# Kernel tuning notes

Measured on AMD Instinct MI355X. Metric: run time of the kernel, lower is better.

## Reference

```python
import jax, jax.numpy as jnp
import numpy as np

# MQIF constants (match init_kwargs / torch defaults)
A = 0.04
B = 0.2
VR = -60.0
VT = -40.0
V_RESET = -60.0
V_PEAK = 30.0
D = 2.0
TAU_M = 10.0
TAU_U = 100.0
DT = 0.05


def setup_inputs() -> dict:
    key = jax.random.key(0)
    input_current = jax.random.normal(key, (16, 4096, 512), dtype=jnp.float32)
    return {"input_current": input_current}


def reference(input_current):
    # input_current: [batch, steps, features]
    batch, steps, features = input_current.shape
    dtype = input_current.dtype
    v0 = jnp.full((batch, features), VR, dtype=dtype)      # v_init defaults to vr
    u0 = jnp.zeros((batch, features), dtype=dtype)          # u_init defaults to 0

    def step(carry, i_t):
        v, u = carry
        fired = v >= V_PEAK
        v_vis = jnp.where(fired, V_PEAK, v)                 # recorded (clamped) voltage at step t
        quad = A * (v - VR) * (v - VT)
        dv = (quad - u + i_t) / TAU_M
        du = (B * (v - VR) - u) / TAU_U
        v_next = jnp.where(fired, V_RESET, v + DT * dv)
        u_next = jnp.where(fired, u + D, u + DT * du)
        return (v_next, u_next), (v_vis, fired)

    # scan over time: [steps, batch, features]
    (v_f, u_f), (v_vis_seq, fired_seq) = jax.lax.scan(
        step, (v0, u0), jnp.swapaxes(input_current, 0, 1)
    )
    v_vis_seq = jnp.swapaxes(v_vis_seq, 0, 1)               # [batch, steps, features]
    fired_seq = jnp.swapaxes(fired_seq, 0, 1)

    # torch semantics: v_trace[:, t] for t<steps is the clamped visible voltage;
    # v_trace[:, steps] is the raw final voltage. spikes[:, t] = (v_t >= v_peak).
    v_trace = jnp.concatenate([v_vis_seq, v_f[:, None, :]], axis=1)   # [batch, steps+1, features]
    spikes = jnp.concatenate([fired_seq, (v_f >= V_PEAK)[:, None, :]], axis=1)
    return v_trace, spikes
```

## Files before the change

kernel.cpp:

```cpp
#include <hip/hip_runtime.h>


#define STEPS 4096
#define FEATS 512
#define BATCH 16
#define CHNK  128
#define NCH   (STEPS / CHNK)
#define SEQ   32

typedef __attribute__((address_space(3))) void lds_void;
typedef __attribute__((address_space(1))) void g_void;

__global__ __launch_bounds__(128, 1)
void mqif_kernel(const float* __restrict__ in,
                 float* __restrict__ vtr,
                 float* __restrict__ spk) {
    constexpr float VPEAK_  = 30.0f;
    constexpr float VRESET_ = -60.0f;
    constexpr float D_      = 2.0f;
    constexpr float C2 = 2.0e-4f;
    constexpr float C1 = 1.02f;
    constexpr float C0 = 0.48f;
    constexpr float DT_TM = 0.005f;
    constexpr float KU  = 1.0f - 5.0e-4f;
    constexpr float KB  = 1.0e-4f;
    constexpr float KBV = 6.0e-3f;

    __shared__ float lds[2][CHNK * SEQ];

    const int tid  = threadIdx.x;
    const int wid  = tid >> 6;
    const int lane = tid & 63;
    const int bid  = blockIdx.x;
    const int b    = bid >> 4;
    const int fb   = (bid & 15) << 5;

    const float* gin = in + (size_t)b * STEPS * FEATS + fb;

    if (wid == 1) {
        const int r  = lane >> 3;
        const int cb = (lane & 7) << 2;
        for (int c = 0; c <= NCH; ++c) {
            if (c < NCH) {
                float* dst = &lds[c & 1][0];
                const float* src = gin + (size_t)c * CHNK * FEATS;
                #pragma unroll
                for (int k = 0; k < (CHNK * SEQ) / 256; ++k) {
                    const float* s = src + (size_t)(k * 8 + r) * FEATS + cb;
                    __builtin_amdgcn_global_load_lds((const g_void*)s,
                                                     (lds_void*)(dst + k * 256),
                                                     16, 0, 0);
                }
            }
            __syncthreads();
        }
        return;
    }

    if (lane >= SEQ) {
        return;
    }

    float* vp = vtr + (size_t)b * (STEPS + 1) * FEATS + fb + lane;
    float* sp = spk + (size_t)b * (STEPS + 1) * FEATS + fb + lane;

    float v = -60.0f;
    float u = 0.0f;

    for (int c = 0; c <= NCH; ++c) {
        if (c >= 1) {
            const float* buf = &lds[(c - 1) & 1][lane];
            const int t0 = (c - 1) * CHNK;
            #pragma unroll 16
            for (int j = 0; j < CHNK; ++j) {
                const float it   = buf[(size_t)j * SEQ];
                const bool fired = (v >= VPEAK_);
                const float vvis = fminf(v, VPEAK_);
                const float sval = fired ? 1.0f : 0.0f;

                const float w  = fmaf(DT_TM, it - u, C0);
                const float p  = fmaf(C2, v, C1);
                const float vn = fmaf(p, v, w);
                const float un = fmaf(KU, u, fmaf(KB, v, KBV));

                __builtin_nontemporal_store(vvis, vp + (size_t)(t0 + j) * FEATS);
                __builtin_nontemporal_store(sval, sp + (size_t)(t0 + j) * FEATS);

                v = fired ? VRESET_ : vn;
                u = fired ? (u + D_) : un;
            }
        }
        __syncthreads();
    }

    __builtin_nontemporal_store(v, vp + (size_t)STEPS * FEATS);
    __builtin_nontemporal_store((v >= VPEAK_) ? 1.0f : 0.0f, sp + (size_t)STEPS * FEATS);
}

extern "C" void kernel_launch(void* const* d_in, const int* in_sizes, int n_in,
                              void* d_out, int out_size, void* d_ws, size_t ws_size,
                              hipStream_t stream) {
    const float* in = (const float*)d_in[0];
    float* vtr = (float*)d_out;
    float* spk = (float*)d_out + (size_t)BATCH * (STEPS + 1) * FEATS;

    dim3 grid(256);
    dim3 block(128);
    mqif_kernel<<<grid, block, 0, stream>>>(in, vtr, spk);
}
```

Baseline: 458.5 us.

## Stage outputs through LDS with dedicated writer waves for vectorized stores

The compute wave now writes the visible voltage and spike values into double-buffered LDS tiles instead of issuing scalar strided global stores. Two extra wavefronts then copy each finished chunk to global memory one chunk behind, using 16-byte vector nontemporal stores. The compute wave also software-prefetches its LDS inputs 16 steps ahead into registers. This takes the global store latency and narrow stores off the serial recurrence path, at the cost of more LDS, a deeper pipeline and an extra barrier iteration.

Measured after the change: 402.0 us. -12.3%, faster.

```diff
diff --git a/kernel.cpp b/kernel.cpp
--- a/kernel.cpp
+++ b/kernel.cpp
@@ -10,8 +10,9 @@
 
 typedef __attribute__((address_space(3))) void lds_void;
 typedef __attribute__((address_space(1))) void g_void;
+typedef float v4f __attribute__((ext_vector_type(4)));
 
-__global__ __launch_bounds__(128, 1)
+__global__ __launch_bounds__(256, 1)
 void mqif_kernel(const float* __restrict__ in,
                  float* __restrict__ vtr,
                  float* __restrict__ spk) {
@@ -26,7 +27,9 @@
     constexpr float KB  = 1.0e-4f;
     constexpr float KBV = 6.0e-3f;
 
-    __shared__ float lds[2][CHNK * SEQ];
+    __shared__ __align__(16) float Lin[2][CHNK * SEQ];
+    __shared__ __align__(16) float Lv [2][CHNK * SEQ];
+    __shared__ __align__(16) float Ls [2][CHNK * SEQ];
 
     const int tid  = threadIdx.x;
     const int wid  = tid >> 6;
@@ -35,66 +38,92 @@
     const int b    = bid >> 4;
     const int fb   = (bid & 15) << 5;
 
-    const float* gin = in + (size_t)b * STEPS * FEATS + fb;
+    const float* gin = in  + (size_t)b * STEPS * FEATS + fb;
+    float*       gv  = vtr + (size_t)b * (STEPS + 1) * FEATS + fb;
+    float*       gs  = spk + (size_t)b * (STEPS + 1) * FEATS + fb;
 
-    if (wid == 1) {
-        const int r  = lane >> 3;
-        const int cb = (lane & 7) << 2;
-        for (int c = 0; c <= NCH; ++c) {
+    const int r  = lane >> 3;
+    const int cb = (lane & 7) << 2;
+
+    float v = -60.0f;
+    float u = 0.0f;
+
+    for (int c = 0; c <= NCH + 1; ++c) {
+        if (wid == 1) {
             if (c < NCH) {
-                float* dst = &lds[c & 1][0];
+                float* dst = &Lin[c & 1][0];
                 const float* src = gin + (size_t)c * CHNK * FEATS;
                 #pragma unroll
-                for (int k = 0; k < (CHNK * SEQ) / 256; ++k) {
+                for (int k = 0; k < 16; ++k) {
                     const float* s = src + (size_t)(k * 8 + r) * FEATS + cb;
                     __builtin_amdgcn_global_load_lds((const g_void*)s,
                                                      (lds_void*)(dst + k * 256),
                                                      16, 0, 0);
                 }
             }
-            __syncthreads();
-        }
-        return;
-    }
+        } else if (wid == 0) {
+            if (c >= 1 && c <= NCH && lane < SEQ) {
+                const int bi = (c - 1) & 1;
+                const float* bin = &Lin[bi][lane];
+                float*       bv  = &Lv [bi][lane];
+                float*       bs  = &Ls [bi][lane];
 
-    if (lane >= SEQ) {
-        return;
-    }
+                float cur[16], nxt[16];
+                #pragma unroll
+                for (int j = 0; j < 16; ++j) cur[j] = bin[j * SEQ];
 
-    float* vp = vtr + (size_t)b * (STEPS + 1) * FEATS + fb + lane;
-    float* sp = spk + (size_t)b * (STEPS + 1) * FEATS + fb + lane;
+                #pragma unroll
+                for (int g = 0; g < 8; ++g) {
+                    if (g < 7) {
+                        #pragma unroll
+                        for (int j = 0; j < 16; ++j)
+                            nxt[j] = bin[(g * 16 + 16 + j) * SEQ];
+                    }
+                    #pragma unroll
+                    for (int j = 0; j < 16; ++j) {
+                        const float it    = cur[j];
+                        const bool  fired = (v >= VPEAK_);
+                        const float vvis  = fminf(v, VPEAK_);
+                        const float sval  = fired ? 1.0f : 0.0f;
 
-    float v = -60.0f;
-    float u = 0.0f;
+                        const float w0 = __builtin_fmaf(-DT_TM, u, C0);
+                        const float w  = __builtin_fmaf(DT_TM, it, w0);
+                        const float p  = __builtin_fmaf(C2, v, C1);
+                        const float vn = __builtin_fmaf(p, v, w);
+                        const float t  = __builtin_fmaf(KB, v, KBV);
+                        const float un = __builtin_fmaf(KU, u, t);
 
-    for (int c = 0; c <= NCH; ++c) {
-        if (c >= 1) {
-            const float* buf = &lds[(c - 1) & 1][lane];
-            const int t0 = (c - 1) * CHNK;
-            #pragma unroll 16
-            for (int j = 0; j < CHNK; ++j) {
-                const float it   = buf[(size_t)j * SEQ];
-                const bool fired = (v >= VPEAK_);
-                const float vvis = fminf(v, VPEAK_);
-                const float sval = fired ? 1.0f : 0.0f;
+                        bv[(g * 16 + j) * SEQ] = vvis;
+                        bs[(g * 16 + j) * SEQ] = sval;
 
-                const float w  = fmaf(DT_TM, it - u, C0);
-                const float p  = fmaf(C2, v, C1);
-                const float vn = fmaf(p, v, w);
-                const float un = fmaf(KU, u, fmaf(KB, v, KBV));
-
-                __builtin_nontemporal_store(vvis, vp + (size_t)(t0 + j) * FEATS);
-                __builtin_nontemporal_store(sval, sp + (size_t)(t0 + j) * FEATS);
-
-                v = fired ? VRESET_ : vn;
-                u = fired ? (u + D_) : un;
+                        v = fired ? VRESET_ : vn;
+                        u = fired ? (u + D_) : un;
+                    }
+                    #pragma unroll
+                    for (int j = 0; j < 16; ++j) cur[j] = nxt[j];
+                }
+            }
+        } else {
+            if (c >= 2) {
+                const int c2 = c - 2;
+                const int bi = c & 1;
+                const float* lsrc = (wid == 2) ? &Lv[bi][0] : &Ls[bi][0];
+                float* gdst = ((wid == 2) ? gv : gs) + (size_t)c2 * CHNK * FEATS;
+                #pragma unroll
+                for (int k = 0; k < 16; ++k) {
+                    const int row = k * 8 + r;
+                    const v4f val = *(const v4f*)&lsrc[(size_t)row * SEQ + cb];
+                    __builtin_nontemporal_store(val, (v4f*)(gdst + (size_t)row * FEATS + cb));
+                }
             }
         }
         __syncthreads();
     }
 
-    __builtin_nontemporal_store(v, vp + (size_t)STEPS * FEATS);
-    __builtin_nontemporal_store((v >= VPEAK_) ? 1.0f : 0.0f, sp + (size_t)STEPS * FEATS);
+    if (wid == 0 && lane < SEQ) {
+        gv[(size_t)STEPS * FEATS + lane] = v;
+        gs[(size_t)STEPS * FEATS + lane] = (v >= VPEAK_) ? 1.0f : 0.0f;
+    }
 }
 
 extern "C" void kernel_launch(void* const* d_in, const int* in_sizes, int n_in,
@@ -105,6 +134,6 @@
     float* spk = (float*)d_out + (size_t)BATCH * (STEPS + 1) * FEATS;
 
     dim3 grid(256);
-    dim3 block(128);
+    dim3 block(256);
     mqif_kernel<<<grid, block, 0, stream>>>(in, vtr, spk);
 }
```
